# Performance work log

Measured on AMD Instinct MI355X. Metric: run time of the kernel, lower is better.

Reference implementation:

```python
import jax, jax.numpy as jnp
import numpy as np

N, FEAT, D, K, L, H, NCLS = 4096, 512, 64, 100, 3, 8, 2
EPS = 1e-15

def _ln(x, g, b, eps=1e-6):
    m = x.mean(-1, keepdims=True)
    v = x.var(-1, keepdims=True)
    return (x - m) * jax.lax.rsqrt(v + eps) * g + b


def setup_inputs():
    key = jax.random.key(0)
    ks = jax.random.split(key, 12)
    w = lambda k, shape: jax.random.normal(k, shape, jnp.float32) * 0.02
    return {
        "node_feat": jax.random.normal(ks[0], (1, N, FEAT), jnp.float32),
        "adj": jax.random.uniform(ks[1], (1, N, N), jnp.float32),
        "conv_w": w(ks[2], (FEAT, D)), "conv_b": jnp.zeros((D,), jnp.float32),
        "bn_g": jnp.ones((D,), jnp.float32), "bn_b": jnp.zeros((D,), jnp.float32),
        "pool_w": w(ks[3], (D, K)), "pool_b": jnp.zeros((K,), jnp.float32),
        "cls_token": jnp.zeros((1, 1, D), jnp.float32),
        "ln1_g": jnp.ones((L, D), jnp.float32), "ln1_b": jnp.zeros((L, D), jnp.float32),
        "qkv_w": w(ks[4], (L, D, 3 * D)), "qkv_b": jnp.zeros((L, 3 * D), jnp.float32),
        "proj_w": w(ks[5], (L, D, D)), "proj_b": jnp.zeros((L, D), jnp.float32),
        "ln2_g": jnp.ones((L, D), jnp.float32), "ln2_b": jnp.zeros((L, D), jnp.float32),
        "fc1_w": w(ks[6], (L, D, 4 * D)), "fc1_b": jnp.zeros((L, 4 * D), jnp.float32),
        "fc2_w": w(ks[7], (L, 4 * D, D)), "fc2_b": jnp.zeros((L, D), jnp.float32),
        "norm_g": jnp.ones((D,), jnp.float32), "norm_b": jnp.zeros((D,), jnp.float32),
        "head_w": w(ks[8], (D, NCLS)), "head_b": jnp.zeros((NCLS,), jnp.float32),
    }


def _forward(node_feat, adj, conv_w, conv_b, bn_g, bn_b, pool_w, pool_b, cls_token,
             ln1_g, ln1_b, qkv_w, qkv_b, proj_w, proj_b, ln2_g, ln2_b,
             fc1_w, fc1_b, fc2_w, fc2_b, norm_g, norm_b, head_w, head_b):
    x = node_feat  # mask is all ones -> X = mask*X is a no-op
    # --- GCNBlock: propagate + self loop + linear + BatchNorm(train stats) + L2 norm ---
    y = jnp.matmul(adj, x) + x                 # [1,N,F]
    y = y @ conv_w + conv_b                    # [1,N,D]
    m = y.mean(axis=(0, 1))
    v = y.var(axis=(0, 1))
    y = (y - m) * jax.lax.rsqrt(v + 1e-5) * bn_g + bn_b
    y = y / jnp.maximum(jnp.linalg.norm(y, axis=2, keepdims=True), 1e-12)
    # --- cluster assignment ---
    s = jax.nn.softmax(y @ pool_w + pool_b, axis=-1)   # [1,N,K]
    # --- dense_mincut_pool ---
    out = jnp.einsum('bnk,bnd->bkd', s, y)             # [1,K,D]
    sa = s[0].T @ adj[0]                               # [K,N] (the torch.sparse.mm)
    out_adj = (sa @ s[0])[None]                        # [1,K,K]
    mincut_num = jnp.trace(out_adj, axis1=1, axis2=2)  # [1]
    d_flat = adj.sum(-1)                               # [1,N] degrees
    # trace(S^T diag(d) S) = sum_i d_i * ||s_i||^2
    mincut_den = jnp.sum(d_flat[0] * jnp.sum(s[0] ** 2, axis=-1))[None]
    mincut_loss = jnp.mean(-(mincut_num / mincut_den))
    ss = jnp.einsum('bnk,bnl->bkl', s, s)
    i_s = jnp.eye(K, dtype=ss.dtype)
    ortho_loss = jnp.mean(jnp.linalg.norm(
        ss / jnp.linalg.norm(ss, axis=(-1, -2), keepdims=True) - i_s / jnp.linalg.norm(i_s),
        axis=(-1, -2)))
    ind = jnp.arange(K)
    out_adj = out_adj.at[:, ind, ind].set(0.0)
    dd = jnp.sqrt(out_adj.sum(-1))[:, None] + EPS      # [1,1,K]
    out_adj = out_adj / dd / jnp.swapaxes(dd, 1, 2)    # (returned by pool; unused downstream)
    # --- transformer over [cls] + K cluster tokens ---
    t = jnp.concatenate([jnp.broadcast_to(cls_token, (1, 1, D)), out], axis=1)  # [1,K+1,D]
    hd = D // H
    scale = hd ** -0.5
    for l in range(L):
        h = _ln(t, ln1_g[l], ln1_b[l])
        qkv = h @ qkv_w[l] + qkv_b[l]
        q, k, vv = jnp.split(qkv, 3, axis=-1)
        sp = lambda a: a.reshape(1, -1, H, hd).transpose(0, 2, 1, 3)
        q, k, vv = sp(q), sp(k), sp(vv)
        att = jax.nn.softmax(jnp.einsum('bhqd,bhkd->bhqk', q, k) * scale, axis=-1)
        o = jnp.einsum('bhqk,bhkd->bhqd', att, vv).transpose(0, 2, 1, 3).reshape(1, -1, D)
        t = t + (o @ proj_w[l] + proj_b[l])
        h = _ln(t, ln2_g[l], ln2_b[l])
        t = t + (jax.nn.gelu(h @ fc1_w[l] + fc1_b[l], approximate=False) @ fc2_w[l] + fc2_b[l])
    t = _ln(t, norm_g, norm_b)
    logits = t[:, 0] @ head_w + head_b                 # [1,NCLS]
    return logits, mincut_loss, ortho_loss


def reference(node_feat, adj, conv_w, conv_b, bn_g, bn_b, pool_w, pool_b, cls_token,
              ln1_g, ln1_b, qkv_w, qkv_b, proj_w, proj_b, ln2_g, ln2_b,
              fc1_w, fc1_b, fc2_w, fc2_b, norm_g, norm_b, head_w, head_b):
    return _forward(node_feat, adj, conv_w, conv_b, bn_g, bn_b, pool_w, pool_b, cls_token,
                    ln1_g, ln1_b, qkv_w, qkv_b, proj_w, proj_b, ln2_g, ln2_b,
                    fc1_w, fc1_b, fc2_w, fc2_b, norm_g, norm_b, head_w, head_b)
```

## Files before the change

kernel.cpp:

```cpp
#include <hip/hip_runtime.h>
#include <hip/hip_bf16.h>
#include <math.h>

#define NN   4096
#define FEAT 512
#define DIM  64
#define KC   100
#define LL   3

#define OFF_DFLAT   0
#define OFF_CHSUM   4096
#define OFF_CHSQ    4160
#define OFF_CTR     4224
#define ZERO_FLOATS 4240
#define OFF_XW      4240
#define OFF_YPART   (OFF_XW + NN*DIM)
#define OFF_GPART   (OFF_YPART + 8*NN*DIM)
#define OFF_Y0      (OFF_GPART + 64*128*192)
#define OFF_QKV     (OFF_Y0 + NN*DIM)
#define OFF_SS      (OFF_QKV + 2*101*192)
#define OFF_DENP    (OFF_SS + KC*KC)
#define OFF_NUMP    (OFF_DENP + 1024)
#define OFF_SB16    (OFF_NUMP + 1024)
#define OFF_STB16   (OFF_SB16 + NN*128/2)
#define OFF_YNT16   (OFF_STB16 + NN*128/2)
#define OFF_XWT16   (OFF_YNT16 + NN*DIM/2)

typedef __attribute__((ext_vector_type(8))) short bfrag;
typedef __attribute__((ext_vector_type(4))) float ffrag;

__device__ __forceinline__ unsigned short f2bf(float f) {
    union { float f; unsigned u; } v; v.f = f;
    return (unsigned short)((v.u + 0x7FFFu + ((v.u >> 16) & 1u)) >> 16);
}
__device__ __forceinline__ float bf2f(unsigned short u) {
    union { unsigned u; float f; } v; v.u = (unsigned)u << 16; return v.f;
}
__device__ __forceinline__ unsigned int pk2(float a, float b) {
    __hip_bfloat162 h = __float22bfloat162_rn(make_float2(a, b));
    return *(unsigned int*)&h;
}

__device__ __forceinline__ float wsum(float v) {
#pragma unroll
    for (int o = 32; o > 0; o >>= 1) v += __shfl_xor(v, o, 64);
    return v;
}
__device__ __forceinline__ float wmax(float v) {
#pragma unroll
    for (int o = 32; o > 0; o >>= 1) v = fmaxf(v, __shfl_xor(v, o, 64));
    return v;
}
__device__ __forceinline__ float hsum32(float v) {
#pragma unroll
    for (int o = 16; o > 0; o >>= 1) v += __shfl_xor(v, o, 64);
    return v;
}
__device__ __forceinline__ float hmax32(float v) {
#pragma unroll
    for (int o = 16; o > 0; o >>= 1) v = fmaxf(v, __shfl_xor(v, o, 64));
    return v;
}

__device__ __forceinline__ unsigned rlx_load(const unsigned* p) {
    return __hip_atomic_load(p, __ATOMIC_RELAXED, __HIP_MEMORY_SCOPE_AGENT);
}
__device__ __forceinline__ void rel_add(unsigned* p) {
    __hip_atomic_fetch_add(p, 1u, __ATOMIC_RELEASE, __HIP_MEMORY_SCOPE_AGENT);
}
template <int SLP>
__device__ __forceinline__ void wait_ge(const unsigned* c, unsigned tgt) {
    while (rlx_load(c) < tgt) __builtin_amdgcn_s_sleep(SLP);
    __builtin_amdgcn_fence(__ATOMIC_ACQUIRE, "agent");
}
__device__ __forceinline__ void gbar(unsigned* c, unsigned tgt) {
    __syncthreads();
    if (threadIdx.x == 0) {
        rel_add(c);
        wait_ge<4>(c, tgt);
    }
    __syncthreads();
}

__global__ __launch_bounds__(256) void xwk(const float* __restrict__ x,
                                           const float* __restrict__ B,
                                           float* __restrict__ xw,
                                           unsigned short* __restrict__ xwT,
                                           float* __restrict__ zws) {
    __shared__ float a_sh[16 * 68];
    __shared__ float b_sh[64 * 68];
    __shared__ unsigned short tl[64 * 17];
    const int t = threadIdx.x, rb = blockIdx.x;
    if (rb < 17) {
        const int zi = rb * 256 + t;
        if (zi < ZERO_FLOATS) zws[zi] = 0.f;
    }
    const int r = t >> 4, cg = (t & 15) * 4;
    float4 acc = make_float4(0.f, 0.f, 0.f, 0.f);
    for (int kt = 0; kt < FEAT; kt += 64) {
        *(float4*)&a_sh[(t >> 4) * 68 + (t & 15) * 4] =
            *(const float4*)(x + (size_t)(rb * 16 + (t >> 4)) * FEAT + kt + (t & 15) * 4);
#pragma unroll
        for (int p = 0; p < 4; ++p) {
            const int idx = t + 256 * p;
            const int kr = idx >> 4, c4 = (idx & 15) * 4;
            *(float4*)&b_sh[kr * 68 + c4] = *(const float4*)(B + (size_t)(kt + kr) * DIM + c4);
        }
        __syncthreads();
#pragma unroll 8
        for (int k = 0; k < 64; ++k) {
            const float av = a_sh[r * 68 + k];
            const float4 bv = *(float4*)&b_sh[k * 68 + cg];
            acc.x += av * bv.x; acc.y += av * bv.y;
            acc.z += av * bv.z; acc.w += av * bv.w;
        }
        __syncthreads();
    }
    *(float4*)&xw[(size_t)(rb * 16 + r) * DIM + cg] = acc;
    tl[(cg + 0) * 17 + r] = f2bf(acc.x);
    tl[(cg + 1) * 17 + r] = f2bf(acc.y);
    tl[(cg + 2) * 17 + r] = f2bf(acc.z);
    tl[(cg + 3) * 17 + r] = f2bf(acc.w);
    __syncthreads();
    const int d = t >> 2, c = (t & 3) * 4;
    ushort4 o;
    o.x = tl[d * 17 + c + 0]; o.y = tl[d * 17 + c + 1];
    o.z = tl[d * 17 + c + 2]; o.w = tl[d * 17 + c + 3];
    *(ushort4*)(xwT + (size_t)d * NN + rb * 16 + c) = o;
}

__global__ __launch_bounds__(256) void gemmA(const float* __restrict__ adj,
                                             const unsigned short* __restrict__ xwT,
                                             float* __restrict__ ypart,
                                             float* __restrict__ dflat) {
    __shared__ __align__(16) unsigned short a_sh[32 * 72];
    __shared__ __align__(16) unsigned short b_sh[64 * 72];
    const int t  = threadIdx.x;
    const int rb = blockIdx.x;
    const int k0 = blockIdx.y * 512;
    const int w = t >> 6, lane = t & 63;
    const int m = lane & 15, q = lane >> 4;
    const int ih = w & 1, jh = w >> 1;
    const int srow = t >> 3, sq = t & 7;
    const int bn = t >> 2, bc = t & 3;
    ffrag acc[2];
    acc[0] = (ffrag){0.f, 0.f, 0.f, 0.f};
    acc[1] = (ffrag){0.f, 0.f, 0.f, 0.f};
    float dacc = 0.f;
    const float* abase = adj + (size_t)(rb * 32 + srow) * NN + k0;
    const unsigned short* bbase = xwT + (size_t)bn * NN + k0;
    for (int kt = 0; kt < 512; kt += 64) {
#pragma unroll
        for (int k = 0; k < 2; ++k) {
            const int p = sq + 8 * k;
            const float4 v = *(const float4*)(abase + kt + 4 * p);
            dacc += v.x + v.y + v.z + v.w;
            *(uint2*)(a_sh + srow * 72 + 4 * p) = make_uint2(pk2(v.x, v.y), pk2(v.z, v.w));
        }
#pragma unroll
        for (int k = 0; k < 2; ++k) {
            const int c2 = bc + 4 * k;
            *(bfrag*)(b_sh + bn * 72 + c2 * 8) = *(const bfrag*)(bbase + kt + c2 * 8);
        }
        __syncthreads();
#pragma unroll
        for (int ks = 0; ks < 2; ++ks) {
            const bfrag af = *(const bfrag*)(a_sh + (ih * 16 + m) * 72 + ks * 32 + q * 8);
#pragma unroll
            for (int jj = 0; jj < 2; ++jj) {
                const bfrag bf = *(const bfrag*)(b_sh + ((jh * 2 + jj) * 16 + m) * 72 + ks * 32 + q * 8);
                acc[jj] = __builtin_amdgcn_mfma_f32_16x16x32_bf16(af, bf, acc[jj], 0, 0, 0);
            }
        }
        __syncthreads();
    }
    float* op = ypart + (size_t)blockIdx.y * NN * DIM;
#pragma unroll
    for (int jj = 0; jj < 2; ++jj)
#pragma unroll
        for (int r = 0; r < 4; ++r)
            op[(size_t)(rb * 32 + ih * 16 + q * 4 + r) * DIM + jh * 32 + jj * 16 + m] = acc[jj][r];
    dacc += __shfl_down(dacc, 1, 64);
    dacc += __shfl_down(dacc, 2, 64);
    dacc += __shfl_down(dacc, 4, 64);
    if (sq == 0) atomicAdd(&dflat[rb * 32 + srow], dacc);
}

__global__ __launch_bounds__(256) void bnstat(const float* __restrict__ ypart,
                                              const float* __restrict__ xw,
                                              const float* __restrict__ conv_b,
                                              float* __restrict__ Y0,
                                              float* __restrict__ chsum,
                                              float* __restrict__ chsq) {
    __shared__ float ssum[64], ssq[64];
    const int t = threadIdx.x;
    if (t < 64) { ssum[t] = 0.f; ssq[t] = 0.f; }
    __syncthreads();
    const int tid = blockIdx.x * 256 + t;
    const size_t e = (size_t)tid * 4;
    const int c0 = (int)(e & 63);
    float4 v = *(const float4*)(xw + e);
#pragma unroll
    for (int s = 0; s < 8; ++s) {
        const float4 u = *(const float4*)(ypart + (size_t)s * NN * DIM + e);
        v.x += u.x; v.y += u.y; v.z += u.z; v.w += u.w;
    }
    const float4 b = *(const float4*)(conv_b + c0);
    v.x += b.x; v.y += b.y; v.z += b.z; v.w += b.w;
    *(float4*)(Y0 + e) = v;
    atomicAdd(&ssum[c0 + 0], v.x); atomicAdd(&ssum[c0 + 1], v.y);
    atomicAdd(&ssum[c0 + 2], v.z); atomicAdd(&ssum[c0 + 3], v.w);
    atomicAdd(&ssq[c0 + 0], v.x * v.x); atomicAdd(&ssq[c0 + 1], v.y * v.y);
    atomicAdd(&ssq[c0 + 2], v.z * v.z); atomicAdd(&ssq[c0 + 3], v.w * v.w);
    __syncthreads();
    if (t < 64) { atomicAdd(&chsum[t], ssum[t]); atomicAdd(&chsq[t], ssq[t]); }
}

__global__ __launch_bounds__(256) void rowsk(const float* __restrict__ Y0,
                                             const float* __restrict__ bn_g,
                                             const float* __restrict__ bn_b,
                                             const float* __restrict__ chsum,
                                             const float* __restrict__ chsq,
                                             const float* __restrict__ pool_w,
                                             const float* __restrict__ pool_b,
                                             const float* __restrict__ dflat,
                                             unsigned short* __restrict__ YnT,
                                             unsigned short* __restrict__ Sb16,
                                             unsigned short* __restrict__ ST,
                                             float* __restrict__ denp) {
    __shared__ float scale_sh[64], shift_sh[64];
    __shared__ float yn_sh[4][64];
    __shared__ float4 pw4[16 * 104];
    __shared__ unsigned short sb_sh[4][128];
    __shared__ float denw[4];
    const int t = threadIdx.x;
    if (t < 64) {
        const float mn  = chsum[t] * (1.f / 4096.f);
        const float var = chsq[t] * (1.f / 4096.f) - mn * mn;
        const float sc  = bn_g[t] * rsqrtf(var + 1e-5f);
        scale_sh[t] = sc;
        shift_sh[t] = bn_b[t] - mn * sc;
    }
    for (int idx = t; idx < 16 * KC; idx += 256) {
        const int dq = idx / KC, k = idx - dq * KC;
        pw4[dq * 104 + k] = make_float4(pool_w[(4 * dq + 0) * KC + k],
                                        pool_w[(4 * dq + 1) * KC + k],
                                        pool_w[(4 * dq + 2) * KC + k],
                                        pool_w[(4 * dq + 3) * KC + k]);
    }
    __syncthreads();
    const int w = t >> 6, lane = t & 63;
    const int row = blockIdx.x * 4 + w;
    float v = Y0[(size_t)row * 64 + lane] * scale_sh[lane] + shift_sh[lane];
    const float nrm = fmaxf(sqrtf(wsum(v * v)), 1e-12f);
    const float yn = v / nrm;
    yn_sh[w][lane] = yn;
    const bool v2 = (lane + 64) < KC;
    const int j2 = v2 ? (lane + 64) : 0;
    float L1 = pool_b[lane];
    float L2 = pool_b[j2];
    __syncthreads();
#pragma unroll
    for (int dq = 0; dq < 16; ++dq) {
        const float4 yv = *(const float4*)&yn_sh[w][4 * dq];
        const float4 w1 = pw4[dq * 104 + lane];
        L1 += yv.x * w1.x + yv.y * w1.y + yv.z * w1.z + yv.w * w1.w;
        const float4 w2 = pw4[dq * 104 + j2];
        L2 += yv.x * w2.x + yv.y * w2.y + yv.z * w2.z + yv.w * w2.w;
    }
    const float mx = wmax(fmaxf(L1, v2 ? L2 : -1e30f));
    const float e1 = expf(L1 - mx);
    const float e2 = v2 ? expf(L2 - mx) : 0.f;
    const float inv = 1.f / wsum(e1 + e2);
    const float s1 = e1 * inv, s2 = e2 * inv;
    const unsigned short b1 = f2bf(s1), b2 = f2bf(s2);
    Sb16[(size_t)row * 128 + lane] = b1;
    Sb16[(size_t)row * 128 + 64 + lane] = b2;
    sb_sh[w][lane] = b1;
    sb_sh[w][64 + lane] = b2;
    const float c = wsum(s1 * s1 + s2 * s2);
    if (lane == 0) denw[w] = dflat[row] * c;
    __syncthreads();
    if (t < 64) {
        ushort4 o;
        o.x = f2bf(yn_sh[0][t]); o.y = f2bf(yn_sh[1][t]);
        o.z = f2bf(yn_sh[2][t]); o.w = f2bf(yn_sh[3][t]);
        *(ushort4*)(YnT + (size_t)t * NN + blockIdx.x * 4) = o;
    } else if (t < 192) {
        const int c2 = t - 64;
        ushort4 o;
        o.x = sb_sh[0][c2]; o.y = sb_sh[1][c2];
        o.z = sb_sh[2][c2]; o.w = sb_sh[3][c2];
        *(ushort4*)(ST + (size_t)c2 * NN + blockIdx.x * 4) = o;
    } else if (t == 192) {
        denp[blockIdx.x] = denw[0] + denw[1] + denw[2] + denw[3];
    }
}

__global__ __launch_bounds__(512) void xform(
        const float* __restrict__ adj,
        const unsigned short* __restrict__ ST,
        const unsigned short* __restrict__ Sb16,
        const unsigned short* __restrict__ YnT,
        float* __restrict__ gpart,
        const float* __restrict__ cls,
        float* __restrict__ ssb,
        float* __restrict__ qkvb,
        const float* __restrict__ g1, const float* __restrict__ b1,
        const float* __restrict__ qw, const float* __restrict__ qb,
        const float* __restrict__ pw, const float* __restrict__ pb,
        const float* __restrict__ g2, const float* __restrict__ b2,
        const float* __restrict__ w1, const float* __restrict__ bb1,
        const float* __restrict__ w2, const float* __restrict__ bb2,
        const float* __restrict__ ng, const float* __restrict__ nb,
        const float* __restrict__ hw, const float* __restrict__ hb,
        const float* __restrict__ denp, float* __restrict__ nump,
        unsigned* __restrict__ ctr,
        float* __restrict__ out) {
    __shared__ __align__(16) float big[13332];
    __shared__ float scsh[8 * 104];
    __shared__ __align__(16) float partf[1056];
    __shared__ float q_l[64], osh[64], h2sh[64], h1sh[64], toksh[64], gsh[256];
    __shared__ float redw8[8];
    float (*part)[132] = (float(*)[132])partf;
    const int t = threadIdx.x, b = blockIdx.x;

    if (b < 101) {
        if (b == 0) {
            if (t < 64) toksh[t] = cls[t];
        } else {
            if (t == 0) wait_ge<2>(&ctr[3], 64u);
            __syncthreads();
            const int row = b - 1;
            if (t < 384) {
                const int col = t % 192, sg = t / 192;
                float v = 0.f;
                const float* gp = gpart + (size_t)row * 192 + col + (size_t)sg * 32 * 24576;
                for (int s = 0; s < 32; ++s) v += gp[(size_t)s * 24576];
                partf[sg * 192 + col] = v;
            }
            __syncthreads();
            if (t < 192) {
                const float v = partf[t] + partf[192 + t];
                if (t < 64) toksh[t] = v;
                else if (t < 164) ssb[row * 100 + (t - 64)] = v;
            }
        }
        __syncthreads();
        if (t < 64) {
            const float x = toksh[t];
            const float m = wsum(x) * (1.f / 64.f);
            const float var = wsum(x * x) * (1.f / 64.f) - m * m;
            h1sh[t] = (x - m) * rsqrtf(var + 1e-6f) * g1[t] + b1[t];
        }
        __syncthreads();
        for (int l = 0; l < LL; ++l) {
            float* qk = qkvb + (size_t)(l & 1) * (101 * 192);
#pragma unroll
            for (int p = 0; p < 6; ++p) {
                const int idx = t + 512 * p;
                ((float4*)big)[idx] = ((const float4*)(qw + (size_t)l * 12288))[idx];
            }
            __syncthreads();
            if (t < 384) {
                const int o = t % 192, grp = t / 192;
                float a = 0.f;
#pragma unroll 8
                for (int e = grp * 32; e < grp * 32 + 32; ++e)
                    a += h1sh[e] * big[e * 192 + o];
                partf[grp * 192 + o] = a;
            }
            __syncthreads();
            if (t < 192)
                qk[b * 192 + t] = qb[l * 192 + t] + partf[t] + partf[192 + t];
            gbar(&ctr[l], 101u);
            float t_old = 0.f;
            if (t < 64) t_old = toksh[t];
#pragma unroll
            for (int p = 0; p < 7; ++p) {
                const int idx = t + 512 * p;
                if (idx < 101 * 32) {
                    const int k = idx >> 5, c = idx & 31;
                    *(float4*)&big[k * 132 + c * 4] = *(const float4*)(qk + k * 192 + 64 + c * 4);
                }
            }
            if (t < 16) *(float4*)&q_l[t * 4] = *(const float4*)(qk + b * 192 + t * 4);
            __syncthreads();
            const float scale = 0.35355339059327373f;
#pragma unroll
            for (int p = 0; p < 2; ++p) {
                const int idx = t + 512 * p;
                if (idx < 808) {
                    const int h = idx / 101, k = idx - h * 101;
                    float s = 0.f;
#pragma unroll
                    for (int d = 0; d < 8; ++d)
                        s += q_l[h * 8 + d] * big[k * 132 + h * 8 + d];
                    scsh[h * 104 + k] = s * scale;
                }
            }
            __syncthreads();
            if (t < 256) {
                const int w = t >> 6;
                const int h = w * 2 + ((t >> 5) & 1);
                const int lft = t & 31;
                float v[4];
#pragma unroll
                for (int g = 0; g < 4; ++g) {
                    const int k = lft + 32 * g;
                    v[g] = (k < 101) ? scsh[h * 104 + k] : -1e30f;
                }
                float mm = fmaxf(fmaxf(v[0], v[1]), fmaxf(v[2], v[3]));
                mm = hmax32(mm);
                float s = 0.f;
#pragma unroll
                for (int g = 0; g < 4; ++g) { v[g] = expf(v[g] - mm); s += v[g]; }
                s = hsum32(s);
                const float inv = 1.f / s;
#pragma unroll
                for (int g = 0; g < 4; ++g) {
                    const int k = lft + 32 * g;
                    if (k < 101) scsh[h * 104 + k] = v[g] * inv;
                }
            }
            __syncthreads();
            {
                const int o = t & 63, grp = t >> 6;
                float po = 0.f;
                for (int k = grp; k < 101; k += 8)
                    po += scsh[(o >> 3) * 104 + k] * big[k * 132 + 64 + o];
                part[grp][o] = po;
            }
            __syncthreads();
            if (t < 64)
                osh[t] = part[0][t] + part[1][t] + part[2][t] + part[3][t]
                       + part[4][t] + part[5][t] + part[6][t] + part[7][t];
            __syncthreads();
#pragma unroll
            for (int p = 0; p < 2; ++p) {
                const int idx = t + 512 * p;
                ((float4*)big)[idx] = ((const float4*)(pw + (size_t)l * 4096))[idx];
            }
            __syncthreads();
            {
                const int o = t & 63, grp = t >> 6;
                float pp = 0.f;
#pragma unroll
                for (int e = grp * 8; e < grp * 8 + 8; ++e)
                    pp += osh[e] * big[e * 64 + o];
                part[grp][o] = pp;
            }
            __syncthreads();
            float t1 = 0.f;
            if (t < 64) {
                float pr = pb[l * 64 + t];
#pragma unroll
                for (int g = 0; g < 8; ++g) pr += part[g][t];
                t1 = t_old + pr;
                const float m = wsum(t1) * (1.f / 64.f);
                const float var = wsum(t1 * t1) * (1.f / 64.f) - m * m;
                h2sh[t] = (t1 - m) * rsqrtf(var + 1e-6f) * g2[l * 64 + t] + b2[l * 64 + t];
            }
            __syncthreads();
            for (int ch = 0; ch < 2; ++ch) {
#pragma unroll
                for (int p = 0; p < 4; ++p) {
                    const int idx = t + 512 * p;
                    const int e = idx >> 5, c = idx & 31;
                    *(float4*)&big[e * 128 + c * 4] =
                        *(const float4*)(w1 + (size_t)l * 16384 + e * 256 + ch * 128 + c * 4);
                }
                __syncthreads();
                {
                    const int o = t & 127, grp = t >> 7;
                    float pa = 0.f;
#pragma unroll
                    for (int e = grp * 16; e < grp * 16 + 16; ++e)
                        pa += h2sh[e] * big[e * 128 + o];
                    part[grp][o] = pa;
                }
                __syncthreads();
                if (t < 128) {
                    float a = bb1[l * 256 + ch * 128 + t]
                            + part[0][t] + part[1][t] + part[2][t] + part[3][t];
                    gsh[ch * 128 + t] = 0.5f * a * (1.f + erff(a * 0.70710678118654752f));
                }
                __syncthreads();
            }
            float a2p = 0.f;
            for (int ch = 0; ch < 2; ++ch) {
#pragma unroll
                for (int p = 0; p < 4; ++p) {
                    const int idx = t + 512 * p;
                    ((float4*)big)[idx] = ((const float4*)(w2 + (size_t)l * 16384 + ch * 8192))[idx];
                }
                __syncthreads();
                {
                    const int o = t & 63, grp = t >> 6;
#pragma unroll
                    for (int er = grp * 16; er < grp * 16 + 16; ++er)
                        a2p += gsh[ch * 128 + er] * big[er * 64 + o];
                }
                __syncthreads();
            }
            {
                const int o = t & 63, grp = t >> 6;
                part[grp][o] = a2p;
            }
            __syncthreads();
            if (t < 64) {
                float a2 = bb2[l * 64 + t];
#pragma unroll
                for (int g = 0; g < 8; ++g) a2 += part[g][t];
                const float tn = t1 + a2;
                toksh[t] = tn;
                if (l < 2) {
                    const float m = wsum(tn) * (1.f / 64.f);
                    const float var = wsum(tn * tn) * (1.f / 64.f) - m * m;
                    h1sh[t] = (tn - m) * rsqrtf(var + 1e-6f) * g1[(l + 1) * 64 + t]
                              + b1[(l + 1) * 64 + t];
                }
            }
            __syncthreads();
        }
        if (b == 0) {
            if (t < 64) {
                const float x = toksh[t];
                const float m = wsum(x) * (1.f / 64.f);
                const float var = wsum(x * x) * (1.f / 64.f) - m * m;
                h1sh[t] = (x - m) * rsqrtf(var + 1e-6f) * ng[t] + nb[t];
            }
            if (t == 0) wait_ge<8>(&ctr[4], 155u);
            __syncthreads();
            float* red = partf;
            red[t] = denp[t] + denp[t + 512];
            __syncthreads();
            for (int s = 256; s > 0; s >>= 1) { if (t < s) red[t] += red[t + s]; __syncthreads(); }
            if (t == 0) q_l[0] = red[0];
            __syncthreads();
            red[t] = nump[t] + nump[t + 512];
            __syncthreads();
            for (int s = 256; s > 0; s >>= 1) { if (t < s) red[t] += red[t + s]; __syncthreads(); }
            if (t == 0) q_l[1] = red[0];
            __syncthreads();
            if (t < 2) {
                float a = hb[t];
                for (int d = 0; d < 64; ++d) a += h1sh[d] * hw[d * 2 + t];
                out[t] = a;
            }
            if (t == 2) out[2] = -(q_l[1] / q_l[0]);
            float s1 = 0.f;
            for (int idx = t; idx < KC * KC; idx += 512) { const float v = ssb[idx]; s1 += v * v; }
            __syncthreads();
            red[t] = s1;
            __syncthreads();
            for (int s = 256; s > 0; s >>= 1) { if (t < s) red[t] += red[t + s]; __syncthreads(); }
            if (t == 0) q_l[2] = sqrtf(red[0]);
            __syncthreads();
            const float inv = 1.f / q_l[2];
            float s2 = 0.f;
            for (int idx = t; idx < KC * KC; idx += 512) {
                float v = ssb[idx] * inv;
                if (idx % 101 == 0) v -= 0.1f;
                s2 += v * v;
            }
            __syncthreads();
            red[t] = s2;
            __syncthreads();
            for (int s = 256; s > 0; s >>= 1) { if (t < s) red[t] += red[t + s]; __syncthreads(); }
            if (t == 0) out[3] = sqrtf(red[0]);
        }
    } else {
        const int wb = b - 101;
        const int w = t >> 6, lane = t & 63;
        const int m = lane & 15, q = lane >> 4;
        if (wb < 64) {
            unsigned short* a_sh = (unsigned short*)big;
            unsigned short* b_sh = (unsigned short*)big + 128 * 72;
            const int k0 = wb * 64;
            const int n0 = t >> 3, c8 = (t & 7) * 8;
#pragma unroll
            for (int p = 0; p < 2; ++p) {
                const int n = n0 + 64 * p;
                *(bfrag*)(a_sh + n * 72 + c8) = *(const bfrag*)(ST + (size_t)n * NN + k0 + c8);
            }
#pragma unroll
            for (int p = 0; p < 3; ++p) {
                const int n = n0 + 64 * p;
                const unsigned short* src = (n < 64) ? (YnT + (size_t)n * NN + k0 + c8)
                                                     : (ST + (size_t)(n - 64) * NN + k0 + c8);
                *(bfrag*)(b_sh + n * 72 + c8) = *(const bfrag*)src;
            }
            __syncthreads();
            ffrag acc[12];
#pragma unroll
            for (int j = 0; j < 12; ++j) acc[j] = (ffrag){0.f, 0.f, 0.f, 0.f};
#pragma unroll
            for (int ks = 0; ks < 2; ++ks) {
                const bfrag af = *(const bfrag*)(a_sh + (w * 16 + m) * 72 + ks * 32 + q * 8);
#pragma unroll
                for (int j = 0; j < 12; ++j) {
                    const bfrag bf = *(const bfrag*)(b_sh + (j * 16 + m) * 72 + ks * 32 + q * 8);
                    acc[j] = __builtin_amdgcn_mfma_f32_16x16x32_bf16(af, bf, acc[j], 0, 0, 0);
                }
            }
            float* op = gpart + (size_t)wb * 128 * 192;
#pragma unroll
            for (int j = 0; j < 12; ++j)
#pragma unroll
                for (int r = 0; r < 4; ++r)
                    op[(size_t)(w * 16 + q * 4 + r) * 192 + j * 16 + m] = acc[j][r];
            __syncthreads();
            if (t == 0) rel_add(&ctr[3]);
        }
        unsigned short* a_sh = (unsigned short*)big;
        unsigned short* s_sh = (unsigned short*)big + 32 * 72;
        const int rh = w & 1, ch = w >> 1;
        const int srow = t >> 4, sq4 = (t & 15) * 4;
        const int sn = t >> 2, scq = t & 3;
        for (int tile = wb; tile < 1024; tile += 155) {
            const int rb = tile & 127;
            const int k0 = (tile >> 7) * 512;
            ffrag acc[2];
            acc[0] = (ffrag){0.f, 0.f, 0.f, 0.f};
            acc[1] = (ffrag){0.f, 0.f, 0.f, 0.f};
            const float* abase = adj + (size_t)(rb * 32 + srow) * NN + k0;
            const unsigned short* sbase = ST + (size_t)sn * NN + k0;
            for (int kt = 0; kt < 512; kt += 64) {
                {
                    const float4 v = *(const float4*)(abase + kt + sq4);
                    *(uint2*)(a_sh + srow * 72 + sq4) = make_uint2(pk2(v.x, v.y), pk2(v.z, v.w));
                }
#pragma unroll
                for (int k = 0; k < 2; ++k) {
                    const int c2 = scq + 4 * k;
                    *(bfrag*)(s_sh + sn * 72 + c2 * 8) = *(const bfrag*)(sbase + kt + c2 * 8);
                }
                __syncthreads();
#pragma unroll
                for (int ks = 0; ks < 2; ++ks) {
                    const bfrag af = *(const bfrag*)(a_sh + (rh * 16 + m) * 72 + ks * 32 + q * 8);
#pragma unroll
                    for (int j = 0; j < 2; ++j) {
                        const bfrag bf = *(const bfrag*)(s_sh + ((ch * 2 + j) * 16 + m) * 72 + ks * 32 + q * 8);
                        acc[j] = __builtin_amdgcn_mfma_f32_16x16x32_bf16(af, bf, acc[j], 0, 0, 0);
                    }
                }
                __syncthreads();
            }
            float local = 0.f;
#pragma unroll
            for (int j = 0; j < 2; ++j)
#pragma unroll
                for (int r = 0; r < 4; ++r) {
                    const int row = rb * 32 + rh * 16 + q * 4 + r;
                    const int col = ch * 32 + j * 16 + m;
                    local += acc[j][r] * bf2f(Sb16[(size_t)row * 128 + col]);
                }
            local = wsum(local);
            if (lane == 0) redw8[w] = local;
            __syncthreads();
            if (t == 0) {
                float s = 0.f;
#pragma unroll
                for (int k = 0; k < 8; ++k) s += redw8[k];
                nump[(tile >> 7) * 128 + rb] = s;
            }
            __syncthreads();
        }
        __syncthreads();
        if (t == 0) rel_add(&ctr[4]);
    }
}

extern "C" void kernel_launch(void* const* d_in, const int* in_sizes, int n_in,
                              void* d_out, int out_size, void* d_ws, size_t ws_size,
                              hipStream_t stream) {
    (void)in_sizes; (void)n_in; (void)out_size; (void)ws_size;
    const float* x      = (const float*)d_in[0];
    const float* adj    = (const float*)d_in[1];
    const float* conv_w = (const float*)d_in[2];
    const float* conv_b = (const float*)d_in[3];
    const float* bn_g   = (const float*)d_in[4];
    const float* bn_b   = (const float*)d_in[5];
    const float* pool_w = (const float*)d_in[6];
    const float* pool_b = (const float*)d_in[7];
    const float* cls    = (const float*)d_in[8];
    const float* ln1_g  = (const float*)d_in[9];
    const float* ln1_b  = (const float*)d_in[10];
    const float* qkv_w  = (const float*)d_in[11];
    const float* qkv_b  = (const float*)d_in[12];
    const float* proj_w = (const float*)d_in[13];
    const float* proj_b = (const float*)d_in[14];
    const float* ln2_g  = (const float*)d_in[15];
    const float* ln2_b  = (const float*)d_in[16];
    const float* fc1_w  = (const float*)d_in[17];
    const float* fc1_b  = (const float*)d_in[18];
    const float* fc2_w  = (const float*)d_in[19];
    const float* fc2_b  = (const float*)d_in[20];
    const float* norm_g = (const float*)d_in[21];
    const float* norm_b = (const float*)d_in[22];
    const float* head_w = (const float*)d_in[23];
    const float* head_b = (const float*)d_in[24];
    float* ws  = (float*)d_ws;
    float* out = (float*)d_out;
    unsigned short* Sb16  = (unsigned short*)(ws + OFF_SB16);
    unsigned short* STb16 = (unsigned short*)(ws + OFF_STB16);
    unsigned short* YnT16 = (unsigned short*)(ws + OFF_YNT16);
    unsigned short* xwT16 = (unsigned short*)(ws + OFF_XWT16);

    xwk<<<256, 256, 0, stream>>>(x, conv_w, ws + OFF_XW, xwT16, ws);
    gemmA<<<dim3(128, 8), 256, 0, stream>>>(adj, xwT16, ws + OFF_YPART, ws + OFF_DFLAT);
    bnstat<<<256, 256, 0, stream>>>(ws + OFF_YPART, ws + OFF_XW, conv_b,
                                    ws + OFF_Y0, ws + OFF_CHSUM, ws + OFF_CHSQ);
    rowsk<<<1024, 256, 0, stream>>>(ws + OFF_Y0, bn_g, bn_b, ws + OFF_CHSUM, ws + OFF_CHSQ,
                                    pool_w, pool_b, ws + OFF_DFLAT,
                                    YnT16, Sb16, STb16, ws + OFF_DENP);
    xform<<<256, 512, 0, stream>>>(adj, STb16, Sb16, YnT16, ws + OFF_GPART, cls,
                                   ws + OFF_SS, ws + OFF_QKV,
                                   ln1_g, ln1_b, qkv_w, qkv_b, proj_w, proj_b,
                                   ln2_g, ln2_b, fc1_w, fc1_b, fc2_w, fc2_b,
                                   norm_g, norm_b, head_w, head_b,
                                   ws + OFF_DENP, ws + OFF_NUMP,
                                   (unsigned*)(ws + OFF_CTR), out);
}
```

Measured before the change: 275.7 us.

## Prefetch transformer weights into registers ahead of use and use lighter barriers

The per-token transformer blocks now issue global loads of the qkv, proj, fc1 and fc2 weights (and the K/V rows) into registers early, so they overlap earlier compute and barriers, and only copy them into shared memory when needed. The next layer's qkv weights are prefetched during the current layer's MLP. Most __syncthreads calls become a custom barrier that waits only on LDS counters (lgkmcnt) rather than all outstanding memory ops, which lets the in-flight global loads cross barriers. This raises register pressure considerably (dozens of float4s live), which could cause spills or lower occupancy.

```diff
diff --git a/kernel.cpp b/kernel.cpp
--- a/kernel.cpp
+++ b/kernel.cpp
@@ -73,13 +73,17 @@
     while (rlx_load(c) < tgt) __builtin_amdgcn_s_sleep(SLP);
     __builtin_amdgcn_fence(__ATOMIC_ACQUIRE, "agent");
 }
+__device__ __forceinline__ void bar() {
+    asm volatile("s_waitcnt lgkmcnt(0)" ::: "memory");
+    __builtin_amdgcn_s_barrier();
+}
 __device__ __forceinline__ void gbar(unsigned* c, unsigned tgt) {
     __syncthreads();
     if (threadIdx.x == 0) {
         rel_add(c);
         wait_ge<4>(c, tgt);
     }
-    __syncthreads();
+    bar();
 }
 
 __global__ __launch_bounds__(256) void xwk(const float* __restrict__ x,
@@ -326,11 +330,17 @@
     const int t = threadIdx.x, b = blockIdx.x;
 
     if (b < 101) {
+        float4 rqkv[6];
+        {
+            const float4* s4 = (const float4*)qw;
+#pragma unroll
+            for (int p = 0; p < 6; ++p) rqkv[p] = s4[t + 512 * p];
+        }
         if (b == 0) {
             if (t < 64) toksh[t] = cls[t];
         } else {
             if (t == 0) wait_ge<2>(&ctr[3], 64u);
-            __syncthreads();
+            bar();
             const int row = b - 1;
             if (t < 384) {
                 const int col = t % 192, sg = t / 192;
@@ -339,29 +349,26 @@
                 for (int s = 0; s < 32; ++s) v += gp[(size_t)s * 24576];
                 partf[sg * 192 + col] = v;
             }
-            __syncthreads();
+            bar();
             if (t < 192) {
                 const float v = partf[t] + partf[192 + t];
                 if (t < 64) toksh[t] = v;
                 else if (t < 164) ssb[row * 100 + (t - 64)] = v;
             }
         }
-        __syncthreads();
+        bar();
         if (t < 64) {
             const float x = toksh[t];
             const float m = wsum(x) * (1.f / 64.f);
             const float var = wsum(x * x) * (1.f / 64.f) - m * m;
             h1sh[t] = (x - m) * rsqrtf(var + 1e-6f) * g1[t] + b1[t];
         }
-        __syncthreads();
+        bar();
         for (int l = 0; l < LL; ++l) {
             float* qk = qkvb + (size_t)(l & 1) * (101 * 192);
 #pragma unroll
-            for (int p = 0; p < 6; ++p) {
-                const int idx = t + 512 * p;
-                ((float4*)big)[idx] = ((const float4*)(qw + (size_t)l * 12288))[idx];
-            }
-            __syncthreads();
+            for (int p = 0; p < 6; ++p) ((float4*)big)[t + 512 * p] = rqkv[p];
+            bar();
             if (t < 384) {
                 const int o = t % 192, grp = t / 192;
                 float a = 0.f;
@@ -370,22 +377,38 @@
                     a += h1sh[e] * big[e * 192 + o];
                 partf[grp * 192 + o] = a;
             }
-            __syncthreads();
+            bar();
             if (t < 192)
                 qk[b * 192 + t] = qb[l * 192 + t] + partf[t] + partf[192 + t];
             gbar(&ctr[l], 101u);
+            float4 rkv[7], rq, rpw[2], rw1a[4];
+#pragma unroll
+            for (int p = 0; p < 7; ++p) {
+                const int idx = t + 512 * p;
+                if (idx < 3232)
+                    rkv[p] = *(const float4*)(qk + (idx >> 5) * 192 + 64 + (idx & 31) * 4);
+            }
+            if (t < 16) rq = *(const float4*)(qk + b * 192 + t * 4);
+#pragma unroll
+            for (int p = 0; p < 2; ++p)
+                rpw[p] = ((const float4*)(pw + (size_t)l * 4096))[t + 512 * p];
+#pragma unroll
+            for (int p = 0; p < 4; ++p) {
+                const int idx = t + 512 * p;
+                rw1a[p] = *(const float4*)(w1 + (size_t)l * 16384 + (idx >> 5) * 256 + (idx & 31) * 4);
+            }
             float t_old = 0.f;
             if (t < 64) t_old = toksh[t];
 #pragma unroll
             for (int p = 0; p < 7; ++p) {
                 const int idx = t + 512 * p;
-                if (idx < 101 * 32) {
+                if (idx < 3232) {
                     const int k = idx >> 5, c = idx & 31;
-                    *(float4*)&big[k * 132 + c * 4] = *(const float4*)(qk + k * 192 + 64 + c * 4);
-                }
-            }
-            if (t < 16) *(float4*)&q_l[t * 4] = *(const float4*)(qk + b * 192 + t * 4);
-            __syncthreads();
+                    *(float4*)&big[k * 132 + c * 4] = rkv[p];
+                }
+            }
+            if (t < 16) *(float4*)&q_l[t * 4] = rq;
+            bar();
             const float scale = 0.35355339059327373f;
 #pragma unroll
             for (int p = 0; p < 2; ++p) {
@@ -399,7 +422,7 @@
                     scsh[h * 104 + k] = s * scale;
                 }
             }
-            __syncthreads();
+            bar();
             if (t < 256) {
                 const int w = t >> 6;
                 const int h = w * 2 + ((t >> 5) & 1);
@@ -423,7 +446,7 @@
                     if (k < 101) scsh[h * 104 + k] = v[g] * inv;
                 }
             }
-            __syncthreads();
+            bar();
             {
                 const int o = t & 63, grp = t >> 6;
                 float po = 0.f;
@@ -431,17 +454,22 @@
                     po += scsh[(o >> 3) * 104 + k] * big[k * 132 + 64 + o];
                 part[grp][o] = po;
             }
-            __syncthreads();
+            bar();
             if (t < 64)
                 osh[t] = part[0][t] + part[1][t] + part[2][t] + part[3][t]
                        + part[4][t] + part[5][t] + part[6][t] + part[7][t];
-            __syncthreads();
-#pragma unroll
-            for (int p = 0; p < 2; ++p) {
+            float4 rw1b[4], rw2a[4], rw2b[4];
+#pragma unroll
+            for (int p = 0; p < 4; ++p) {
                 const int idx = t + 512 * p;
-                ((float4*)big)[idx] = ((const float4*)(pw + (size_t)l * 4096))[idx];
-            }
-            __syncthreads();
+                rw1b[p] = *(const float4*)(w1 + (size_t)l * 16384 + (idx >> 5) * 256 + 128 + (idx & 31) * 4);
+                rw2a[p] = ((const float4*)(w2 + (size_t)l * 16384))[idx];
+                rw2b[p] = ((const float4*)(w2 + (size_t)l * 16384 + 8192))[idx];
+            }
+            bar();
+#pragma unroll
+            for (int p = 0; p < 2; ++p) ((float4*)big)[t + 512 * p] = rpw[p];
+            bar();
             {
                 const int o = t & 63, grp = t >> 6;
                 float pp = 0.f;
@@ -450,7 +478,7 @@
                     pp += osh[e] * big[e * 64 + o];
                 part[grp][o] = pp;
             }
-            __syncthreads();
+            bar();
             float t1 = 0.f;
             if (t < 64) {
                 float pr = pb[l * 64 + t];
@@ -461,53 +489,80 @@
                 const float var = wsum(t1 * t1) * (1.f / 64.f) - m * m;
                 h2sh[t] = (t1 - m) * rsqrtf(var + 1e-6f) * g2[l * 64 + t] + b2[l * 64 + t];
             }
-            __syncthreads();
-            for (int ch = 0; ch < 2; ++ch) {
-#pragma unroll
-                for (int p = 0; p < 4; ++p) {
-                    const int idx = t + 512 * p;
-                    const int e = idx >> 5, c = idx & 31;
-                    *(float4*)&big[e * 128 + c * 4] =
-                        *(const float4*)(w1 + (size_t)l * 16384 + e * 256 + ch * 128 + c * 4);
-                }
-                __syncthreads();
-                {
-                    const int o = t & 127, grp = t >> 7;
-                    float pa = 0.f;
-#pragma unroll
-                    for (int e = grp * 16; e < grp * 16 + 16; ++e)
-                        pa += h2sh[e] * big[e * 128 + o];
-                    part[grp][o] = pa;
-                }
-                __syncthreads();
-                if (t < 128) {
-                    float a = bb1[l * 256 + ch * 128 + t]
-                            + part[0][t] + part[1][t] + part[2][t] + part[3][t];
-                    gsh[ch * 128 + t] = 0.5f * a * (1.f + erff(a * 0.70710678118654752f));
-                }
-                __syncthreads();
-            }
+            bar();
+#pragma unroll
+            for (int p = 0; p < 4; ++p) {
+                const int idx = t + 512 * p;
+                *(float4*)&big[(idx >> 5) * 128 + (idx & 31) * 4] = rw1a[p];
+            }
+            bar();
+            {
+                const int o = t & 127, grp = t >> 7;
+                float pa = 0.f;
+#pragma unroll
+                for (int e = grp * 16; e < grp * 16 + 16; ++e)
+                    pa += h2sh[e] * big[e * 128 + o];
+                part[grp][o] = pa;
+            }
+            bar();
+            if (t < 128) {
+                float a = bb1[l * 256 + t]
+                        + part[0][t] + part[1][t] + part[2][t] + part[3][t];
+                gsh[t] = 0.5f * a * (1.f + erff(a * 0.70710678118654752f));
+            }
+            bar();
+#pragma unroll
+            for (int p = 0; p < 4; ++p) {
+                const int idx = t + 512 * p;
+                *(float4*)&big[(idx >> 5) * 128 + (idx & 31) * 4] = rw1b[p];
+            }
+            bar();
+            {
+                const int o = t & 127, grp = t >> 7;
+                float pa = 0.f;
+#pragma unroll
+                for (int e = grp * 16; e < grp * 16 + 16; ++e)
+                    pa += h2sh[e] * big[e * 128 + o];
+                part[grp][o] = pa;
+            }
+            bar();
+            if (t < 128) {
+                float a = bb1[l * 256 + 128 + t]
+                        + part[0][t] + part[1][t] + part[2][t] + part[3][t];
+                gsh[128 + t] = 0.5f * a * (1.f + erff(a * 0.70710678118654752f));
+            }
+            bar();
             float a2p = 0.f;
-            for (int ch = 0; ch < 2; ++ch) {
-#pragma unroll
-                for (int p = 0; p < 4; ++p) {
-                    const int idx = t + 512 * p;
-                    ((float4*)big)[idx] = ((const float4*)(w2 + (size_t)l * 16384 + ch * 8192))[idx];
-                }
-                __syncthreads();
-                {
-                    const int o = t & 63, grp = t >> 6;
-#pragma unroll
-                    for (int er = grp * 16; er < grp * 16 + 16; ++er)
-                        a2p += gsh[ch * 128 + er] * big[er * 64 + o];
-                }
-                __syncthreads();
-            }
+#pragma unroll
+            for (int p = 0; p < 4; ++p) ((float4*)big)[t + 512 * p] = rw2a[p];
+            bar();
+            {
+                const int o = t & 63, grp = t >> 6;
+#pragma unroll
+                for (int er = grp * 16; er < grp * 16 + 16; ++er)
+                    a2p += gsh[er] * big[er * 64 + o];
+            }
+            bar();
+#pragma unroll
+            for (int p = 0; p < 4; ++p) ((float4*)big)[t + 512 * p] = rw2b[p];
+            bar();
+            {
+                const int o = t & 63, grp = t >> 6;
+#pragma unroll
+                for (int er = grp * 16; er < grp * 16 + 16; ++er)
+                    a2p += gsh[128 + er] * big[er * 64 + o];
+            }
+            if (l < 2) {
+                const float4* s4 = (const float4*)(qw + (size_t)(l + 1) * 12288);
+#pragma unroll
+                for (int p = 0; p < 6; ++p) rqkv[p] = s4[t + 512 * p];
+            }
+            bar();
             {
                 const int o = t & 63, grp = t >> 6;
                 part[grp][o] = a2p;
             }
-            __syncthreads();
+            bar();
             if (t < 64) {
                 float a2 = bb2[l * 64 + t];
 #pragma unroll
@@ -521,7 +576,7 @@
                               + b1[(l + 1) * 64 + t];
                 }
             }
-            __syncthreads();
+            bar();
         }
         if (b == 0) {
             if (t < 64) {
```

Result: slower. 290.3 us (+5.3%).

## Read transformer weights directly, lighten barriers, and register-prefetch the adjacency tiles

Applied to the files above, without the earlier changes.

The transformer token blocks now read the QKV, proj, fc1 and fc2 weights and the K/V rows straight from global memory instead of staging them in shared memory, which drops many staging loops and barriers. __syncthreads is replaced by a lighter barrier that waits only on LDS counters, and the global wait gains an explicit vmcnt drain. The adjacency-times-assignment MFMA loop is rewritten with a two-deep register prefetch, so global loads for the next tile overlap with compute. The risks are uncoalesced or redundant global weight reads from every block, and memory-ordering hazards from the weaker barrier.

```diff
diff --git a/kernel.cpp b/kernel.cpp
--- a/kernel.cpp
+++ b/kernel.cpp
@@ -72,6 +72,11 @@
 __device__ __forceinline__ void wait_ge(const unsigned* c, unsigned tgt) {
     while (rlx_load(c) < tgt) __builtin_amdgcn_s_sleep(SLP);
     __builtin_amdgcn_fence(__ATOMIC_ACQUIRE, "agent");
+    asm volatile("s_waitcnt vmcnt(0)" ::: "memory");
+}
+__device__ __forceinline__ void bar() {
+    asm volatile("s_waitcnt lgkmcnt(0)" ::: "memory");
+    __builtin_amdgcn_s_barrier();
 }
 __device__ __forceinline__ void gbar(unsigned* c, unsigned tgt) {
     __syncthreads();
@@ -79,7 +84,7 @@
         rel_add(c);
         wait_ge<4>(c, tgt);
     }
-    __syncthreads();
+    bar();
 }
 
 __global__ __launch_bounds__(256) void xwk(const float* __restrict__ x,
@@ -330,7 +335,7 @@
             if (t < 64) toksh[t] = cls[t];
         } else {
             if (t == 0) wait_ge<2>(&ctr[3], 64u);
-            __syncthreads();
+            bar();
             const int row = b - 1;
             if (t < 384) {
                 const int col = t % 192, sg = t / 192;
@@ -339,67 +344,54 @@
                 for (int s = 0; s < 32; ++s) v += gp[(size_t)s * 24576];
                 partf[sg * 192 + col] = v;
             }
-            __syncthreads();
+            bar();
             if (t < 192) {
                 const float v = partf[t] + partf[192 + t];
                 if (t < 64) toksh[t] = v;
                 else if (t < 164) ssb[row * 100 + (t - 64)] = v;
             }
         }
-        __syncthreads();
+        bar();
         if (t < 64) {
             const float x = toksh[t];
             const float m = wsum(x) * (1.f / 64.f);
             const float var = wsum(x * x) * (1.f / 64.f) - m * m;
             h1sh[t] = (x - m) * rsqrtf(var + 1e-6f) * g1[t] + b1[t];
         }
-        __syncthreads();
+        bar();
         for (int l = 0; l < LL; ++l) {
             float* qk = qkvb + (size_t)(l & 1) * (101 * 192);
-#pragma unroll
-            for (int p = 0; p < 6; ++p) {
-                const int idx = t + 512 * p;
-                ((float4*)big)[idx] = ((const float4*)(qw + (size_t)l * 12288))[idx];
-            }
-            __syncthreads();
             if (t < 384) {
                 const int o = t % 192, grp = t / 192;
+                const float* wp = qw + (size_t)l * 12288 + grp * 32 * 192 + o;
                 float a = 0.f;
-#pragma unroll 8
-                for (int e = grp * 32; e < grp * 32 + 32; ++e)
-                    a += h1sh[e] * big[e * 192 + o];
+#pragma unroll
+                for (int e = 0; e < 32; ++e) a += h1sh[grp * 32 + e] * wp[e * 192];
                 partf[grp * 192 + o] = a;
             }
-            __syncthreads();
+            bar();
             if (t < 192)
                 qk[b * 192 + t] = qb[l * 192 + t] + partf[t] + partf[192 + t];
             gbar(&ctr[l], 101u);
             float t_old = 0.f;
             if (t < 64) t_old = toksh[t];
-#pragma unroll
-            for (int p = 0; p < 7; ++p) {
-                const int idx = t + 512 * p;
-                if (idx < 101 * 32) {
-                    const int k = idx >> 5, c = idx & 31;
-                    *(float4*)&big[k * 132 + c * 4] = *(const float4*)(qk + k * 192 + 64 + c * 4);
-                }
-            }
             if (t < 16) *(float4*)&q_l[t * 4] = *(const float4*)(qk + b * 192 + t * 4);
-            __syncthreads();
+            bar();
             const float scale = 0.35355339059327373f;
 #pragma unroll
             for (int p = 0; p < 2; ++p) {
                 const int idx = t + 512 * p;
                 if (idx < 808) {
                     const int h = idx / 101, k = idx - h * 101;
+                    const float* kp = qk + k * 192 + 64 + h * 8;
                     float s = 0.f;
 #pragma unroll
                     for (int d = 0; d < 8; ++d)
-                        s += q_l[h * 8 + d] * big[k * 132 + h * 8 + d];
+                        s += q_l[h * 8 + d] * kp[d];
                     scsh[h * 104 + k] = s * scale;
                 }
             }
-            __syncthreads();
+            bar();
             if (t < 256) {
                 const int w = t >> 6;
                 const int h = w * 2 + ((t >> 5) & 1);
@@ -423,34 +415,28 @@
                     if (k < 101) scsh[h * 104 + k] = v[g] * inv;
                 }
             }
-            __syncthreads();
+            bar();
             {
                 const int o = t & 63, grp = t >> 6;
                 float po = 0.f;
                 for (int k = grp; k < 101; k += 8)
-                    po += scsh[(o >> 3) * 104 + k] * big[k * 132 + 64 + o];
+                    po += scsh[(o >> 3) * 104 + k] * qk[k * 192 + 128 + o];
                 part[grp][o] = po;
             }
-            __syncthreads();
+            bar();
             if (t < 64)
                 osh[t] = part[0][t] + part[1][t] + part[2][t] + part[3][t]
                        + part[4][t] + part[5][t] + part[6][t] + part[7][t];
-            __syncthreads();
-#pragma unroll
-            for (int p = 0; p < 2; ++p) {
-                const int idx = t + 512 * p;
-                ((float4*)big)[idx] = ((const float4*)(pw + (size_t)l * 4096))[idx];
-            }
-            __syncthreads();
+            bar();
             {
                 const int o = t & 63, grp = t >> 6;
+                const float* wp = pw + (size_t)l * 4096 + grp * 8 * 64 + o;
                 float pp = 0.f;
 #pragma unroll
-                for (int e = grp * 8; e < grp * 8 + 8; ++e)
-                    pp += osh[e] * big[e * 64 + o];
+                for (int e = 0; e < 8; ++e) pp += osh[grp * 8 + e] * wp[e * 64];
                 part[grp][o] = pp;
             }
-            __syncthreads();
+            bar();
             float t1 = 0.f;
             if (t < 64) {
                 float pr = pb[l * 64 + t];
@@ -461,53 +447,30 @@
                 const float var = wsum(t1 * t1) * (1.f / 64.f) - m * m;
                 h2sh[t] = (t1 - m) * rsqrtf(var + 1e-6f) * g2[l * 64 + t] + b2[l * 64 + t];
             }
-            __syncthreads();
-            for (int ch = 0; ch < 2; ++ch) {
-#pragma unroll
-                for (int p = 0; p < 4; ++p) {
-                    const int idx = t + 512 * p;
-                    const int e = idx >> 5, c = idx & 31;
-                    *(float4*)&big[e * 128 + c * 4] =
-                        *(const float4*)(w1 + (size_t)l * 16384 + e * 256 + ch * 128 + c * 4);
-                }
-                __syncthreads();
-                {
-                    const int o = t & 127, grp = t >> 7;
-                    float pa = 0.f;
-#pragma unroll
-                    for (int e = grp * 16; e < grp * 16 + 16; ++e)
-                        pa += h2sh[e] * big[e * 128 + o];
-                    part[grp][o] = pa;
-                }
-                __syncthreads();
-                if (t < 128) {
-                    float a = bb1[l * 256 + ch * 128 + t]
-                            + part[0][t] + part[1][t] + part[2][t] + part[3][t];
-                    gsh[ch * 128 + t] = 0.5f * a * (1.f + erff(a * 0.70710678118654752f));
-                }
-                __syncthreads();
-            }
-            float a2p = 0.f;
-            for (int ch = 0; ch < 2; ++ch) {
-#pragma unroll
-                for (int p = 0; p < 4; ++p) {
-                    const int idx = t + 512 * p;
-                    ((float4*)big)[idx] = ((const float4*)(w2 + (size_t)l * 16384 + ch * 8192))[idx];
-                }
-                __syncthreads();
-                {
-                    const int o = t & 63, grp = t >> 6;
-#pragma unroll
-                    for (int er = grp * 16; er < grp * 16 + 16; ++er)
-                        a2p += gsh[ch * 128 + er] * big[er * 64 + o];
-                }
-                __syncthreads();
-            }
+            bar();
+            {
+                const int o = t & 255, grp = t >> 8;
+                const float* wp = w1 + (size_t)l * 16384 + grp * 32 * 256 + o;
+                float pa = 0.f;
+#pragma unroll
+                for (int e = 0; e < 32; ++e) pa += h2sh[grp * 32 + e] * wp[e * 256];
+                partf[grp * 256 + o] = pa;
+            }
+            bar();
+            if (t < 256) {
+                float a = bb1[l * 256 + t] + partf[t] + partf[256 + t];
+                gsh[t] = 0.5f * a * (1.f + erff(a * 0.70710678118654752f));
+            }
+            bar();
             {
                 const int o = t & 63, grp = t >> 6;
+                const float* wp = w2 + (size_t)l * 16384 + grp * 32 * 64 + o;
+                float a2p = 0.f;
+#pragma unroll
+                for (int er = 0; er < 32; ++er) a2p += gsh[grp * 32 + er] * wp[er * 64];
                 part[grp][o] = a2p;
             }
-            __syncthreads();
+            bar();
             if (t < 64) {
                 float a2 = bb2[l * 64 + t];
 #pragma unroll
@@ -521,7 +484,7 @@
                               + b1[(l + 1) * 64 + t];
                 }
             }
-            __syncthreads();
+            bar();
         }
         if (b == 0) {
             if (t < 64) {
@@ -626,17 +589,23 @@
             acc[1] = (ffrag){0.f, 0.f, 0.f, 0.f};
             const float* abase = adj + (size_t)(rb * 32 + srow) * NN + k0;
             const unsigned short* sbase = ST + (size_t)sn * NN + k0;
-            for (int kt = 0; kt < 512; kt += 64) {
-                {
-                    const float4 v = *(const float4*)(abase + kt + sq4);
-                    *(uint2*)(a_sh + srow * 72 + sq4) = make_uint2(pk2(v.x, v.y), pk2(v.z, v.w));
-                }
-#pragma unroll
-                for (int k = 0; k < 2; ++k) {
-                    const int c2 = scq + 4 * k;
-                    *(bfrag*)(s_sh + sn * 72 + c2 * 8) = *(const bfrag*)(sbase + kt + c2 * 8);
-                }
-                __syncthreads();
+            float4 av_a = *(const float4*)(abase + sq4);
+            bfrag sa0 = *(const bfrag*)(sbase + scq * 8);
+            bfrag sa1 = *(const bfrag*)(sbase + (scq + 4) * 8);
+            float4 av_b = *(const float4*)(abase + 64 + sq4);
+            bfrag sb0 = *(const bfrag*)(sbase + 64 + scq * 8);
+            bfrag sb1 = *(const bfrag*)(sbase + 64 + (scq + 4) * 8);
+#pragma unroll
+            for (int kt = 0; kt < 512; kt += 128) {
+                *(uint2*)(a_sh + srow * 72 + sq4) = make_uint2(pk2(av_a.x, av_a.y), pk2(av_a.z, av_a.w));
+                *(bfrag*)(s_sh + sn * 72 + scq * 8) = sa0;
+                *(bfrag*)(s_sh + sn * 72 + (scq + 4) * 8) = sa1;
+                if (kt + 128 < 512) {
+                    av_a = *(const float4*)(abase + kt + 128 + sq4);
+                    sa0  = *(const bfrag*)(sbase + kt + 128 + scq * 8);
+                    sa1  = *(const bfrag*)(sbase + kt + 128 + (scq + 4) * 8);
+                }
+                bar();
 #pragma unroll
                 for (int ks = 0; ks < 2; ++ks) {
                     const bfrag af = *(const bfrag*)(a_sh + (rh * 16 + m) * 72 + ks * 32 + q * 8);
@@ -646,7 +615,26 @@
                         acc[j] = __builtin_amdgcn_mfma_f32_16x16x32_bf16(af, bf, acc[j], 0, 0, 0);
                     }
                 }
-                __syncthreads();
+                bar();
+                *(uint2*)(a_sh + srow * 72 + sq4) = make_uint2(pk2(av_b.x, av_b.y), pk2(av_b.z, av_b.w));
+                *(bfrag*)(s_sh + sn * 72 + scq * 8) = sb0;
+                *(bfrag*)(s_sh + sn * 72 + (scq + 4) * 8) = sb1;
+                if (kt + 192 < 512) {
+                    av_b = *(const float4*)(abase + kt + 192 + sq4);
+                    sb0  = *(const bfrag*)(sbase + kt + 192 + scq * 8);
+                    sb1  = *(const bfrag*)(sbase + kt + 192 + (scq + 4) * 8);
+                }
+                bar();
+#pragma unroll
+                for (int ks = 0; ks < 2; ++ks) {
+                    const bfrag af = *(const bfrag*)(a_sh + (rh * 16 + m) * 72 + ks * 32 + q * 8);
+#pragma unroll
+                    for (int j = 0; j < 2; ++j) {
+                        const bfrag bf = *(const bfrag*)(s_sh + ((ch * 2 + j) * 16 + m) * 72 + ks * 32 + q * 8);
+                        acc[j] = __builtin_amdgcn_mfma_f32_16x16x32_bf16(af, bf, acc[j], 0, 0, 0);
+                    }
+                }
+                bar();
             }
             float local = 0.f;
 #pragma unroll
@@ -659,14 +647,13 @@
                 }
             local = wsum(local);
             if (lane == 0) redw8[w] = local;
-            __syncthreads();
+            bar();
             if (t == 0) {
                 float s = 0.f;
 #pragma unroll
                 for (int k = 0; k < 8; ++k) s += redw8[k];
                 nump[(tile >> 7) * 128 + rb] = s;
             }
-            __syncthreads();
         }
         __syncthreads();
         if (t == 0) rel_add(&ctr[4]);
```

After: 258.5 us. 1.07x faster.
